# Performance work log

Measured on AMD Instinct MI355X. Metric: run time of the kernel, lower is better.

## Reference

```python
import jax, jax.numpy as jnp
import numpy as np
import math

COND_DIM = 64
HIDDEN = 128
NUM_SIN = 2
SQRT2 = 1.4142135623730951


def fused_leaky_relu(x, bias):
    # stylegan2 fused bias + leaky relu (slope 0.2) with sqrt(2) gain
    return jax.nn.leaky_relu(x + bias, negative_slope=0.2) * SQRT2


def equal_linear2(x, W, b, lr_mul=1.0, activation=False):
    scale = lr_mul / math.sqrt(W.shape[1])
    out = x @ (W * scale).T
    if activation:
        return fused_leaky_relu(out, b * lr_mul)
    return out + b * lr_mul


def coords_to_sinusoidals(x, num_sinusoidals=NUM_SIN, multiplier=2.0):
    # x: [P, 1] -> [P, 2*num_sinusoidals], freq_type='mult': freqs = multiplier**i
    freqs = multiplier ** jnp.arange(num_sinusoidals, dtype=x.dtype)  # [S]
    ang = x * freqs  # [P, S]
    return jnp.concatenate([jnp.sin(ang), jnp.cos(ang)], axis=-1)


def setup_inputs() -> dict:
    key = jax.random.key(0)
    ks = jax.random.split(key, 10)
    B, N = 64, 8192
    coord_in = 2 * NUM_SIN  # 4
    in1 = coord_in + COND_DIM  # 68
    in2 = HIDDEN + COND_DIM    # 192
    coords = jax.random.normal(ks[0], (B, N, 2), dtype=jnp.float32)
    c = jax.random.normal(ks[1], (B, N, COND_DIM), dtype=jnp.float32)
    # EqualLinear2 weights init uniform(-1,1)/lr_mul; last layer zero in torch,
    # use small random values here so gradients/outputs are non-trivial.
    Wx1 = jax.random.uniform(ks[2], (HIDDEN, in1), minval=-1.0, maxval=1.0)
    bx1 = jnp.zeros((HIDDEN,), jnp.float32)
    Wx2 = jax.random.uniform(ks[3], (2, in2), minval=-1.0, maxval=1.0) * 0.1
    bx2 = jnp.zeros((2,), jnp.float32)
    Wy1 = jax.random.uniform(ks[4], (HIDDEN, in1), minval=-1.0, maxval=1.0)
    by1 = jnp.zeros((HIDDEN,), jnp.float32)
    Wy2 = jax.random.uniform(ks[5], (2, in2), minval=-1.0, maxval=1.0) * 0.1
    by2 = jnp.zeros((2,), jnp.float32)
    return {"coords": coords, "c": c,
            "Wx1": Wx1, "bx1": bx1, "Wx2": Wx2, "bx2": bx2,
            "Wy1": Wy1, "by1": by1, "Wy2": Wy2, "by2": by2}


def reference(coords, c, Wx1, bx1, Wx2, bx2, Wy1, by1, Wy2, by2):
    initial_shape = coords.shape[:-1]
    coords2 = coords.reshape(-1, coords.shape[-1])  # [P, 2]
    cf = c.reshape(-1, c.shape[-1])                 # [P, cond]
    x = coords2[:, 0:1]
    y = coords2[:, 1:2]

    # x branch -> affine params for y
    h = coords_to_sinusoidals(x / 10.0)
    h = equal_linear2(jnp.concatenate([h, cf], -1), Wx1, bx1, activation=True)
    o = equal_linear2(jnp.concatenate([h, cf], -1), Wx2, bx2, activation=False)
    y_log_scale = jnp.clip(o[:, 0:1], -5.0, 5.0)
    y_bias = o[:, 1:2]
    y = y * jnp.exp(y_log_scale) + y_bias

    # y branch -> affine params for x
    h = coords_to_sinusoidals(y / 10.0)
    h = equal_linear2(jnp.concatenate([h, cf], -1), Wy1, by1, activation=True)
    o = equal_linear2(jnp.concatenate([h, cf], -1), Wy2, by2, activation=False)
    x_log_scale = jnp.clip(o[:, 0:1], -5.0, 5.0)
    x_bias = o[:, 1:2]
    x = x * jnp.exp(x_log_scale) + x_bias

    warped = jnp.concatenate([x, y], -1).reshape(*initial_shape, -1)
    log_jac = jnp.concatenate([x_log_scale + y_log_scale], -1)
    log_jac = (x_log_scale + y_log_scale).reshape(*initial_shape, -1)
    return warped, log_jac
```

## Files before the change

kernel.cpp:

```cpp
#include <hip/hip_runtime.h>

typedef unsigned short u16t;
typedef short short8 __attribute__((ext_vector_type(8)));
typedef float f32x4 __attribute__((ext_vector_type(4)));

__device__ __forceinline__ u16t f2bf_rne(float f) {
  unsigned u = __builtin_bit_cast(unsigned, f);
  u += 0x7FFFu + ((u >> 16) & 1u);
  return (u16t)(u >> 16);
}
__device__ __forceinline__ unsigned pk2(float a, float b) {
  unsigned ua = __builtin_bit_cast(unsigned, a) + 0x8000u;
  unsigned ub = __builtin_bit_cast(unsigned, b) + 0x8000u;
  return (ua >> 16) | (ub & 0xFFFF0000u);
}
union S8U { short8 s; unsigned w[4]; };
__device__ __forceinline__ short8 pack8f(float4 a, float4 b) {
  S8U u;
  u.w[0] = pk2(a.x, a.y); u.w[1] = pk2(a.z, a.w);
  u.w[2] = pk2(b.x, b.y); u.w[3] = pk2(b.z, b.w);
  return u.s;
}

#define WS_WB  0
#define WS_BS  32768
#define WS_FF  34816
#define WS_BC  38912
#define LDS_BYTES 38912
#define WS_BYTES 43008

__global__ void prep_kernel(const float* __restrict__ Wx1, const float* __restrict__ bx1,
                            const float* __restrict__ Wx2,
                            const float* __restrict__ Wy1, const float* __restrict__ by1,
                            const float* __restrict__ Wy2,
                            char* __restrict__ ws)
{
  const int b = blockIdx.x;
  const int lane = threadIdx.x;
  const int p = b >> 3, nt = b & 7;
  const int l15 = lane & 15, quad = lane >> 4;
  const float* W1 = p ? Wy1 : Wx1;
  const float* B1 = p ? by1 : bx1;
  const float* W2 = p ? Wy2 : Wx2;
  const int n = nt * 16 + l15;
  const float* rp = W1 + n * 68;
  short8 bb0, bb1;
  #pragma unroll
  for (int j = 0; j < 8; ++j) {
    bb0[j] = (short)f2bf_rne(rp[4 + quad * 8 + j]);
    bb1[j] = (short)f2bf_rne(rp[36 + quad * 8 + j]);
  }
  short8* wb = (short8*)(ws + WS_WB);
  wb[((p * 8 + nt) * 2 + 0) * 64 + lane] = bb0;
  wb[((p * 8 + nt) * 2 + 1) * 64 + lane] = bb1;

  if (quad == 0) {
    uint2 t;
    t.x = (unsigned)f2bf_rne(rp[0]) | ((unsigned)f2bf_rne(rp[1]) << 16);
    t.y = (unsigned)f2bf_rne(rp[2]) | ((unsigned)f2bf_rne(rp[3]) << 16);
    ((uint2*)(ws + WS_BS))[(p * 8 + nt) * 16 + l15] = t;
  }

  if (lane < 16) {
    const float SQ2 = 1.41421356237309515f;
    const int nn = nt * 16 + lane;
    float4 ff;
    ff.x = B1[nn]; ff.y = W2[nn] * SQ2; ff.z = W2[192 + nn] * SQ2; ff.w = 0.f;
    ((float4*)(ws + WS_FF))[(p * 8 + nt) * 16 + lane] = ff;
  }

  if (b < 4) {
    const int p2 = b >> 1, h = b & 1;
    const float* W2b = p2 ? Wy2 : Wx2;
    short8 bc = (short8)0;
    if (l15 < 2) {
      #pragma unroll
      for (int j = 0; j < 8; ++j)
        bc[j] = (short)f2bf_rne(W2b[l15 * 192 + 128 + h * 32 + quad * 8 + j]);
    }
    ((short8*)(ws + WS_BC))[(p2 * 2 + h) * 64 + lane] = bc;
  }
}

__global__ __launch_bounds__(512, 2)
void icb_main(const float* __restrict__ g_coords, const float* __restrict__ g_c,
              const float* __restrict__ g_bx2, const float* __restrict__ g_by2,
              const char* __restrict__ ws, float* __restrict__ g_out)
{
  __shared__ float4 s_tab4[LDS_BYTES / 16];
  char* s_tab = (char*)s_tab4;

  const int tid  = threadIdx.x;
  const int lane = tid & 63, wave = tid >> 6;
  const int l15  = lane & 15, quad = lane >> 4;
  const int wbase = blockIdx.x * 256 + wave * 32;

  float4 ra[2][4]; float2 rco[2];
  #pragma unroll
  for (int mt = 0; mt < 2; ++mt) {
    const int r = wbase + mt * 16 + l15;
    const float4* cr = (const float4*)(g_c + (size_t)r * 64);
    ra[mt][0] = cr[quad * 2];     ra[mt][1] = cr[quad * 2 + 1];
    ra[mt][2] = cr[8 + quad * 2]; ra[mt][3] = cr[8 + quad * 2 + 1];
    rco[mt] = ((const float2*)g_coords)[r];
  }

  {
    const float4* src = (const float4*)ws;
    #pragma unroll
    for (int k = 0; k < 5; ++k) {
      const int t = tid + k * 512;
      if (t < LDS_BYTES / 16) s_tab4[t] = src[t];
    }
  }

  short8 aC0[2], aC1[2];
  float xold[2], yold[2];
  #pragma unroll
  for (int mt = 0; mt < 2; ++mt) {
    aC0[mt] = pack8f(ra[mt][0], ra[mt][1]);
    aC1[mt] = pack8f(ra[mt][2], ra[mt][3]);
    xold[mt] = rco[mt].x; yold[mt] = rco[mt].y;
  }

  __syncthreads();

  const short8* wb  = (const short8*)(s_tab + WS_WB);
  const uint2*  wbs = (const uint2*) (s_tab + WS_BS);
  const float4* wf  = (const float4*)(s_tab + WS_FF);
  const short8* wbc = (const short8*)(ws + WS_BC);

  const float s1 = 0.121267812518166f;
  const float s2 = 0.0721687836487032f;

  float vin[2], xnew[2], ynew[2], xls[2], yls[2];
  vin[0] = xold[0]; vin[1] = xold[1];

  #pragma unroll 1
  for (int path = 0; path < 2; ++path) {
    const int pb = path * 8;
    const float* b2 = path ? g_by2 : g_bx2;
    const float b20 = b2[0], b21 = b2[1];

    short8 aS[2];
    #pragma unroll
    for (int mt = 0; mt < 2; ++mt) {
      short8 f = (short8)0;
      if (quad == 0) {
        float a = vin[mt] * 0.1f;
        float sa, ca;
        __sincosf(a, &sa, &ca);
        float s2a = 2.0f * sa * ca;
        float c2a = 1.0f - 2.0f * sa * sa;
        f[0] = (short)f2bf_rne(sa); f[1] = (short)f2bf_rne(s2a);
        f[2] = (short)f2bf_rne(ca); f[3] = (short)f2bf_rne(c2a);
      }
      aS[mt] = f;
    }

    short8 bc0 = wbc[(path * 2 + 0) * 64 + lane];
    short8 bc1 = wbc[(path * 2 + 1) * 64 + lane];
    f32x4 acc8[2];
    #pragma unroll
    for (int mt = 0; mt < 2; ++mt) {
      f32x4 a = {0.f, 0.f, 0.f, 0.f};
      a = __builtin_amdgcn_mfma_f32_16x16x32_bf16(aC0[mt], bc0, a, 0, 0, 0);
      a = __builtin_amdgcn_mfma_f32_16x16x32_bf16(aC1[mt], bc1, a, 0, 0, 0);
      acc8[mt] = a;
    }

    float hp[2][4][2];
    #pragma unroll
    for (int mt = 0; mt < 2; ++mt)
      #pragma unroll
      for (int j = 0; j < 4; ++j) { hp[mt][j][0] = 0.f; hp[mt][j][1] = 0.f; }

    #pragma unroll 2
    for (int nt = 0; nt < 8; ++nt) {
      short8 bb0 = wb[((pb + nt) * 2 + 0) * 64 + lane];
      short8 bb1 = wb[((pb + nt) * 2 + 1) * 64 + lane];
      uint2  bsv = wbs[(pb + nt) * 16 + l15];
      S8U su; su.w[0] = bsv.x; su.w[1] = bsv.y; su.w[2] = bsv.x; su.w[3] = bsv.y;
      const short8 bs = su.s;
      float4 ff  = wf[(pb + nt) * 16 + l15];
      #pragma unroll
      for (int mt = 0; mt < 2; ++mt) {
        f32x4 acc = {0.f, 0.f, 0.f, 0.f};
        acc = __builtin_amdgcn_mfma_f32_16x16x32_bf16(aC0[mt], bb0, acc, 0, 0, 0);
        acc = __builtin_amdgcn_mfma_f32_16x16x32_bf16(aC1[mt], bb1, acc, 0, 0, 0);
        acc = __builtin_amdgcn_mfma_f32_16x16x32_bf16(aS[mt],  bs,  acc, 0, 0, 0);
        #pragma unroll
        for (int j = 0; j < 4; ++j) {
          float v = fmaf(s1, acc[j], ff.x);
          float h = fmaxf(v, 0.2f * v);
          hp[mt][j][0] = fmaf(h, ff.y, hp[mt][j][0]);
          hp[mt][j][1] = fmaf(h, ff.z, hp[mt][j][1]);
        }
      }
    }

    #pragma unroll
    for (int mt = 0; mt < 2; ++mt)
      #pragma unroll
      for (int j = 0; j < 4; ++j) {
        hp[mt][j][0] += (l15 == 0) ? acc8[mt][j] : 0.f;
        hp[mt][j][1] += (l15 == 1) ? acc8[mt][j] : 0.f;
      }

    #pragma unroll
    for (int mt = 0; mt < 2; ++mt)
      #pragma unroll
      for (int j = 0; j < 4; ++j)
        #pragma unroll
        for (int o = 0; o < 2; ++o) {
          float v = hp[mt][j][o];
          v += __shfl_xor(v, 1);
          v += __shfl_xor(v, 2);
          v += __shfl_xor(v, 4);
          v += __shfl_xor(v, 8);
          hp[mt][j][o] = v;
        }

    const int jm = l15 & 3;
    const int src = ((l15 >> 2) << 4) | jm;
    #pragma unroll
    for (int mt = 0; mt < 2; ++mt) {
      float t0[4], t1[4];
      #pragma unroll
      for (int j = 0; j < 4; ++j) {
        t0[j] = fmaf(s2, hp[mt][j][0], b20);
        t1[j] = fmaf(s2, hp[mt][j][1], b21);
      }
      float s0 = (jm & 1) ? t0[1] : t0[0], s0b = (jm & 1) ? t0[3] : t0[2];
      s0 = (jm & 2) ? s0b : s0;
      float s1v = (jm & 1) ? t1[1] : t1[0], s1b = (jm & 1) ? t1[3] : t1[2];
      s1v = (jm & 2) ? s1b : s1v;
      float lsraw = __shfl(s0, src);
      float brow  = __shfl(s1v, src);

      float ls = fminf(fmaxf(lsraw, -5.f), 5.f);
      float e  = __expf(ls);
      if (path == 0) {
        yls[mt]  = ls;
        ynew[mt] = fmaf(yold[mt], e, brow);
        vin[mt]  = ynew[mt];
      } else {
        xls[mt]  = ls;
        xnew[mt] = fmaf(xold[mt], e, brow);
      }
    }
  }

  if (lane < 16) {
    #pragma unroll
    for (int mt = 0; mt < 2; ++mt) {
      int R = wbase + mt * 16 + lane;
      float2 pw; pw.x = xnew[mt]; pw.y = ynew[mt];
      reinterpret_cast<float2*>(g_out)[R] = pw;
      g_out[1048576 + R] = xls[mt] + yls[mt];
    }
  }
}

extern "C" void kernel_launch(void* const* d_in, const int* in_sizes, int n_in,
                              void* d_out, int out_size, void* d_ws, size_t ws_size,
                              hipStream_t stream) {
  (void)in_sizes; (void)n_in; (void)out_size; (void)ws_size;
  prep_kernel<<<16, 64, 0, stream>>>(
      (const float*)d_in[2], (const float*)d_in[3], (const float*)d_in[4],
      (const float*)d_in[6], (const float*)d_in[7], (const float*)d_in[8],
      (char*)d_ws);
  icb_main<<<2048, 512, 0, stream>>>(
      (const float*)d_in[0], (const float*)d_in[1],
      (const float*)d_in[5], (const float*)d_in[9],
      (const char*)d_ws, (float*)d_out);
}
```

Before: 234.3 us.

## Swap MFMA operand order so hidden units run along rows, shrinking reductions

```diff
diff --git a/kernel.cpp b/kernel.cpp
--- a/kernel.cpp
+++ b/kernel.cpp
@@ -24,10 +24,10 @@
 
 #define WS_WB  0
 #define WS_BS  32768
-#define WS_FF  34816
-#define WS_BC  38912
-#define LDS_BYTES 38912
-#define WS_BYTES 43008
+#define WS_FQ  36864
+#define LDS_BYTES 39936
+#define WS_BC  39936
+#define WS_BYTES 44032
 
 __global__ void prep_kernel(const float* __restrict__ Wx1, const float* __restrict__ bx1,
                             const float* __restrict__ Wx2,
@@ -55,18 +55,23 @@
   wb[((p * 8 + nt) * 2 + 1) * 64 + lane] = bb1;
 
   if (quad == 0) {
-    uint2 t;
-    t.x = (unsigned)f2bf_rne(rp[0]) | ((unsigned)f2bf_rne(rp[1]) << 16);
-    t.y = (unsigned)f2bf_rne(rp[2]) | ((unsigned)f2bf_rne(rp[3]) << 16);
-    ((uint2*)(ws + WS_BS))[(p * 8 + nt) * 16 + l15] = t;
-  }
-
-  if (lane < 16) {
+    short8 t = (short8)0;
+    #pragma unroll
+    for (int j = 0; j < 4; ++j) t[j] = (short)f2bf_rne(rp[j]);
+    ((short8*)(ws + WS_BS))[(p * 8 + nt) * 16 + l15] = t;
+  }
+
+  if (lane < 12) {
+    const int q = lane / 3, t = lane - q * 3;
     const float SQ2 = 1.41421356237309515f;
-    const int nn = nt * 16 + lane;
-    float4 ff;
-    ff.x = B1[nn]; ff.y = W2[nn] * SQ2; ff.z = W2[192 + nn] * SQ2; ff.w = 0.f;
-    ((float4*)(ws + WS_FF))[(p * 8 + nt) * 16 + lane] = ff;
+    float4 v;
+    #pragma unroll
+    for (int j = 0; j < 4; ++j) {
+      const int nn = nt * 16 + q * 4 + j;
+      float val = (t == 0) ? B1[nn] : (t == 1) ? W2[nn] * SQ2 : W2[192 + nn] * SQ2;
+      ((float*)&v)[j] = val;
+    }
+    ((float4*)(ws + WS_FQ))[((p * 8 + nt) * 4 + q) * 3 + t] = v;
   }
 
   if (b < 4) {
@@ -126,8 +131,8 @@
   __syncthreads();
 
   const short8* wb  = (const short8*)(s_tab + WS_WB);
-  const uint2*  wbs = (const uint2*) (s_tab + WS_BS);
-  const float4* wf  = (const float4*)(s_tab + WS_FF);
+  const short8* wbs = (const short8*)(s_tab + WS_BS);
+  const float4* wfq = (const float4*)(s_tab + WS_FQ);
   const short8* wbc = (const short8*)(ws + WS_BC);
 
   const float s1 = 0.121267812518166f;
@@ -164,80 +169,50 @@
     #pragma unroll
     for (int mt = 0; mt < 2; ++mt) {
       f32x4 a = {0.f, 0.f, 0.f, 0.f};
-      a = __builtin_amdgcn_mfma_f32_16x16x32_bf16(aC0[mt], bc0, a, 0, 0, 0);
-      a = __builtin_amdgcn_mfma_f32_16x16x32_bf16(aC1[mt], bc1, a, 0, 0, 0);
+      a = __builtin_amdgcn_mfma_f32_16x16x32_bf16(bc0, aC0[mt], a, 0, 0, 0);
+      a = __builtin_amdgcn_mfma_f32_16x16x32_bf16(bc1, aC1[mt], a, 0, 0, 0);
       acc8[mt] = a;
     }
 
-    float hp[2][4][2];
-    #pragma unroll
-    for (int mt = 0; mt < 2; ++mt)
-      #pragma unroll
-      for (int j = 0; j < 4; ++j) { hp[mt][j][0] = 0.f; hp[mt][j][1] = 0.f; }
+    float hp[2][2] = {{0.f, 0.f}, {0.f, 0.f}};
 
     #pragma unroll 2
     for (int nt = 0; nt < 8; ++nt) {
       short8 bb0 = wb[((pb + nt) * 2 + 0) * 64 + lane];
       short8 bb1 = wb[((pb + nt) * 2 + 1) * 64 + lane];
-      uint2  bsv = wbs[(pb + nt) * 16 + l15];
-      S8U su; su.w[0] = bsv.x; su.w[1] = bsv.y; su.w[2] = bsv.x; su.w[3] = bsv.y;
-      const short8 bs = su.s;
-      float4 ff  = wf[(pb + nt) * 16 + l15];
+      short8 bsw = wbs[(pb + nt) * 16 + l15];
+      const float4* fq = wfq + ((pb + nt) * 4 + quad) * 3;
+      float4 b1q = fq[0], w0q = fq[1], w1q = fq[2];
       #pragma unroll
       for (int mt = 0; mt < 2; ++mt) {
         f32x4 acc = {0.f, 0.f, 0.f, 0.f};
-        acc = __builtin_amdgcn_mfma_f32_16x16x32_bf16(aC0[mt], bb0, acc, 0, 0, 0);
-        acc = __builtin_amdgcn_mfma_f32_16x16x32_bf16(aC1[mt], bb1, acc, 0, 0, 0);
-        acc = __builtin_amdgcn_mfma_f32_16x16x32_bf16(aS[mt],  bs,  acc, 0, 0, 0);
+        acc = __builtin_amdgcn_mfma_f32_16x16x32_bf16(bb0, aC0[mt], acc, 0, 0, 0);
+        acc = __builtin_amdgcn_mfma_f32_16x16x32_bf16(bb1, aC1[mt], acc, 0, 0, 0);
+        acc = __builtin_amdgcn_mfma_f32_16x16x32_bf16(bsw, aS[mt],  acc, 0, 0, 0);
         #pragma unroll
         for (int j = 0; j < 4; ++j) {
-          float v = fmaf(s1, acc[j], ff.x);
+          float v = fmaf(s1, acc[j], ((const float*)&b1q)[j]);
           float h = fmaxf(v, 0.2f * v);
-          hp[mt][j][0] = fmaf(h, ff.y, hp[mt][j][0]);
-          hp[mt][j][1] = fmaf(h, ff.z, hp[mt][j][1]);
+          hp[mt][0] = fmaf(h, ((const float*)&w0q)[j], hp[mt][0]);
+          hp[mt][1] = fmaf(h, ((const float*)&w1q)[j], hp[mt][1]);
         }
       }
     }
 
     #pragma unroll
-    for (int mt = 0; mt < 2; ++mt)
-      #pragma unroll
-      for (int j = 0; j < 4; ++j) {
-        hp[mt][j][0] += (l15 == 0) ? acc8[mt][j] : 0.f;
-        hp[mt][j][1] += (l15 == 1) ? acc8[mt][j] : 0.f;
-      }
-
-    #pragma unroll
-    for (int mt = 0; mt < 2; ++mt)
-      #pragma unroll
-      for (int j = 0; j < 4; ++j)
-        #pragma unroll
-        for (int o = 0; o < 2; ++o) {
-          float v = hp[mt][j][o];
-          v += __shfl_xor(v, 1);
-          v += __shfl_xor(v, 2);
-          v += __shfl_xor(v, 4);
-          v += __shfl_xor(v, 8);
-          hp[mt][j][o] = v;
-        }
-
-    const int jm = l15 & 3;
-    const int src = ((l15 >> 2) << 4) | jm;
-    #pragma unroll
-    for (int mt = 0; mt < 2; ++mt) {
-      float t0[4], t1[4];
-      #pragma unroll
-      for (int j = 0; j < 4; ++j) {
-        t0[j] = fmaf(s2, hp[mt][j][0], b20);
-        t1[j] = fmaf(s2, hp[mt][j][1], b21);
-      }
-      float s0 = (jm & 1) ? t0[1] : t0[0], s0b = (jm & 1) ? t0[3] : t0[2];
-      s0 = (jm & 2) ? s0b : s0;
-      float s1v = (jm & 1) ? t1[1] : t1[0], s1b = (jm & 1) ? t1[3] : t1[2];
-      s1v = (jm & 2) ? s1b : s1v;
-      float lsraw = __shfl(s0, src);
-      float brow  = __shfl(s1v, src);
-
+    for (int mt = 0; mt < 2; ++mt) {
+      hp[mt][0] += acc8[mt][0];
+      hp[mt][1] += acc8[mt][1];
+    }
+
+    #pragma unroll
+    for (int mt = 0; mt < 2; ++mt) {
+      float h0 = hp[mt][0], h1 = hp[mt][1];
+      h0 += __shfl_xor(h0, 16); h0 += __shfl_xor(h0, 32);
+      h1 += __shfl_xor(h1, 16); h1 += __shfl_xor(h1, 32);
+
+      float lsraw = fmaf(s2, h0, b20);
+      float brow  = fmaf(s2, h1, b21);
       float ls = fminf(fmaxf(lsraw, -5.f), 5.f);
       float e  = __expf(ls);
       if (path == 0) {
```

Measured after the change: 228.2 us. 1.03x faster.
